# Kernel optimization log

Measured on AMD Instinct MI355X. Metric: run time of the kernel, lower is better.

## Reference

```python
import jax, jax.numpy as jnp
import numpy as np
from jax import lax

L, B, S, D, H = 4, 4, 2048, 1024, 2048
EPS = 1e-5


def setup_inputs() -> dict:
    key = jax.random.key(0)
    ks = jax.random.split(key, 8)

    def rn(k, shape, fan_in, fan_out):
        scale = (2.0 / (fan_in + fan_out)) ** 0.5  # xavier-ish
        return jax.random.normal(k, shape, jnp.float32) * scale

    return {
        "x": jax.random.normal(ks[0], (B, S, D), jnp.float32),
        "Wp1": rn(ks[1], (L, H, D), D, H),
        "bp1": jnp.zeros((L, H), jnp.float32),
        "Wp2": rn(ks[2], (L, H, D), D, H),
        "bp2": jnp.zeros((L, H), jnp.float32),
        "convW": rn(ks[3], (L, H, H, 3), 3 * H, H),  # torch Conv1d layout (O, I, K)
        "convb": jnp.zeros((L, H), jnp.float32),
        "Wz": rn(ks[4], (L, H, H), H, H),
        "bz": jnp.zeros((L, H), jnp.float32),
        "Wh": rn(ks[5], (L, H, H), H, H),
        "bh": jnp.zeros((L, H), jnp.float32),
        "Wd": rn(ks[6], (L, D, H), H, D),
        "bd": jnp.zeros((L, D), jnp.float32),
        # 4 LayerNorms per layer: [strand1_ln1, conv_ln, gru_ln, strand2_ln1]
        "ln_g": jnp.ones((L, 4, H), jnp.float32),
        "ln_b": jnp.zeros((L, 4, H), jnp.float32),
    }


def _ln(x, g, b):
    m = jnp.mean(x, axis=-1, keepdims=True)
    xc = x - m
    v = jnp.mean(xc * xc, axis=-1, keepdims=True)
    return xc * lax.rsqrt(v + EPS) * g + b


def _log_g(x):
    return jnp.where(x >= 0, jnp.log(jax.nn.relu(x) + 0.5), -jax.nn.softplus(-x))


def _min_gru(x, Wz, bz, Wh, bh):
    # x: (B, S, H); training-mode log-space parallel scan, h_0 = 0
    k = jnp.einsum('bsh,oh->bso', x, Wz) + bz
    log_z = -jax.nn.softplus(-k)
    log_coeffs = -jax.nn.softplus(k)
    log_h0 = jnp.full((x.shape[0], 1, Wz.shape[0]), jnp.log(0.5), x.dtype)  # log_g(0)
    log_tilde_h = _log_g(jnp.einsum('bsh,oh->bso', x, Wh) + bh)
    log_values = jnp.concatenate([log_h0, log_z + log_tilde_h], axis=1)  # (B,S+1,H)
    a_star = jnp.pad(jnp.cumsum(log_coeffs, axis=1), ((0, 0), (1, 0), (0, 0)))
    log_h = a_star + lax.cumlogsumexp(log_values - a_star, axis=1)
    return jnp.exp(log_h)[:, 1:]


def _conv1d(x, w, b):
    # x: (B, S, H) -> NCH conv with kernel 3, same padding
    y = lax.conv_general_dilated(
        x.transpose(0, 2, 1), w, window_strides=(1,), padding=((1, 1),),
        dimension_numbers=('NCH', 'OIH', 'NCH'))
    return (y + b[None, :, None]).transpose(0, 2, 1)


def _forward(x, Wp1, bp1, Wp2, bp2, convW, convb, Wz, bz, Wh, bh, Wd, bd, ln_g, ln_b):
    for i in range(L):
        s1 = _ln(jnp.einsum('bsd,hd->bsh', x, Wp1[i]) + bp1[i], ln_g[i, 0], ln_b[i, 0])
        s1 = _ln(_conv1d(s1, convW[i], convb[i]), ln_g[i, 1], ln_b[i, 1])
        s1 = jax.nn.silu(s1)
        s1 = _min_gru(s1, Wz[i], bz[i], Wh[i], bh[i])
        s1 = _ln(s1, ln_g[i, 2], ln_b[i, 2])
        s2 = jax.nn.silu(_ln(jnp.einsum('bsd,hd->bsh', x, Wp2[i]) + bp2[i], ln_g[i, 3], ln_b[i, 3]))
        x = jnp.einsum('bsh,dh->bsd', s1 * s2, Wd[i]) + bd[i] + x
    return x


def reference(x, Wp1, bp1, Wp2, bp2, convW, convb, Wz, bz, Wh, bh, Wd, bd, ln_g, ln_b):
    return _forward(x, Wp1, bp1, Wp2, bp2, convW, convb, Wz, bz, Wh, bh, Wd, bd, ln_g, ln_b)
```

## Files before the change

kernel.cpp:

```cpp
#include <hip/hip_runtime.h>

typedef unsigned short u16;
typedef short  s16x8 __attribute__((ext_vector_type(8)));
typedef float  f32x4 __attribute__((ext_vector_type(4)));
typedef unsigned short u16x4 __attribute__((ext_vector_type(4)));

#define LDS_AS __attribute__((address_space(3)))
#define GLB_AS __attribute__((address_space(1)))

__device__ __forceinline__ float bf2f(u16 x) {
    unsigned u = ((unsigned)x) << 16;
    return __builtin_bit_cast(float, u);
}
__device__ __forceinline__ u16 f2bf(float f) {
    unsigned u = __builtin_bit_cast(unsigned, f);
    return (u16)((u + 0x7FFFu + ((u >> 16) & 1u)) >> 16);
}
__device__ __forceinline__ void gload16(const u16* g, u16* l) {
    __builtin_amdgcn_global_load_lds((const GLB_AS unsigned int*)g,
                                     (LDS_AS unsigned int*)l, 16, 0, 0);
}

static constexpr int Lc = 4, Sc = 2048, Dc = 1024, Hc = 2048, Mc = 8192;
static constexpr int CH = 64, CL = 32;
static constexpr int NCHAN = 4 * Hc;

#define BAR() __builtin_amdgcn_s_barrier()
#define VMCNT(n) asm volatile("s_waitcnt vmcnt(" #n ")" ::: "memory")

#define READ_A(d, BUF, MH)                                                     \
    _Pragma("unroll") for (int mf = 0; mf < 4; ++mf) {                         \
        d[mf][0] = *(const s16x8*)(aB0 + (BUF)*16384 + (MH)*4096 + mf*1024);   \
        d[mf][1] = *(const s16x8*)(aB1 + (BUF)*16384 + (MH)*4096 + mf*1024);   \
    }
#define READ_B(BUF, NH)                                                        \
    _Pragma("unroll") for (int jb = 0; jb < 2; ++jb) {                         \
        bq[jb][0] = *(const s16x8*)(bB0 + (BUF)*16384 + (NH)*2048 + jb*1024);  \
        bq[jb][1] = *(const s16x8*)(bB1 + (BUF)*16384 + (NH)*2048 + jb*1024);  \
    }
#define QUAD(a, MH, NH)                                                        \
    _Pragma("unroll") for (int mf = 0; mf < 4; ++mf)                           \
    _Pragma("unroll") for (int jb = 0; jb < 2; ++jb)                           \
    _Pragma("unroll") for (int kk = 0; kk < 2; ++kk)                           \
        acc[(MH)*4 + mf][(NH)*2 + jb] = __builtin_amdgcn_mfma_f32_16x16x32_bf16( \
            a[mf][kk], bq[jb][kk], acc[(MH)*4 + mf][(NH)*2 + jb], 0, 0, 0);

#define STAGE_A(BUF, H, KT) {                                                  \
    if (CONV) {                                                                \
        const int seg_ = ((KT)*64) >> 11;                                      \
        const int kb_  = ((KT)*64) & (Hc - 1);                                 \
        const int r0_  = convRow + (H)*128 + seg_;                             \
        const u16* s0_ = ((unsigned)(r0_ - bb) < (unsigned)Sc)                 \
                             ? A + (size_t)r0_ * lda + kb_ + scol : zerobuf;   \
        const u16* s1_ = ((unsigned)(r0_ + 8 - bb) < (unsigned)Sc)             \
                             ? A + (size_t)(r0_ + 8) * lda + kb_ + scol : zerobuf; \
        gload16(s0_, ldsA + (BUF)*16384 + (H)*8192);                           \
        gload16(s1_, ldsA + (BUF)*16384 + (H)*8192 + 512);                     \
    } else {                                                                   \
        const u16* s_ = srcA + (size_t)((H)*128) * lda + (KT)*64;              \
        gload16(s_,                   ldsA + (BUF)*16384 + (H)*8192);          \
        gload16(s_ + 8*(size_t)lda,   ldsA + (BUF)*16384 + (H)*8192 + 512);    \
    } }
#define STAGE_B(BUF, H, KT) {                                                  \
    const u16* s_ = srcB + (size_t)((H)*128) * K + (KT)*64;                    \
    gload16(s_,                 ldsB + (BUF)*16384 + (H)*8192);                \
    gload16(s_ + 8*(size_t)K,   ldsB + (BUF)*16384 + (H)*8192 + 512);          \
}

template <int CONV>
__global__ __launch_bounds__(512, 2)
void gemm8(const u16* __restrict__ A, const u16* __restrict__ Bw,
           const float* __restrict__ bias, u16* __restrict__ Cb,
           int M, int N, int K, int lda, const u16* __restrict__ zerobuf) {
    (void)M;
    __shared__ __align__(16) u16 As[2][256][64];
    __shared__ __align__(16) u16 Bs[2][256][64];

    const int tid = threadIdx.x;
    const int w = tid >> 6, l = tid & 63;
    const int wm = w & 1, wn = w >> 1;
    const int rowBase = blockIdx.y * 256;
    const int colBase = blockIdx.x * 256;

    const int srow = w * 16 + (l >> 3);
    const int scol = ((l & 7) ^ (l >> 3)) << 3;
    const u16* srcB = Bw + (size_t)(colBase + srow) * K + scol;
    const u16* srcA = A + (size_t)(rowBase + srow) * lda + scol;
    u16* const ldsA = &As[0][0][0] + w * 1024;
    u16* const ldsB = &Bs[0][0][0] + w * 1024;
    const int bb = rowBase & ~(Sc - 1);
    const int convRow = rowBase + srow - 1;

    const int r16 = l & 15, slot = l >> 4;
    const int swz = (r16 & 7) << 4;
    const int co0 = (((slot << 4)      ) ^ swz) >> 1;
    const int co1 = (((slot << 4) | 64 ) ^ swz) >> 1;
    const u16* aB0 = &As[0][0][0] + (wm * 128 + r16) * 64 + co0;
    const u16* aB1 = &As[0][0][0] + (wm * 128 + r16) * 64 + co1;
    const u16* bB0 = &Bs[0][0][0] + (wn * 64  + r16) * 64 + co0;
    const u16* bB1 = &Bs[0][0][0] + (wn * 64  + r16) * 64 + co1;

    f32x4 acc[8][4];
#pragma unroll
    for (int m = 0; m < 8; ++m)
#pragma unroll
        for (int n = 0; n < 4; ++n)
#pragma unroll
            for (int r = 0; r < 4; ++r) acc[m][n][r] = 0.f;

    s16x8 a0[4][2], a1[4][2], bq[2][2];

    STAGE_A(0, 0, 0); STAGE_A(0, 1, 0); STAGE_B(0, 0, 0); STAGE_B(0, 1, 0);
    VMCNT(4);
    STAGE_A(1, 0, 1); STAGE_A(1, 1, 1); STAGE_B(1, 0, 1);
    VMCNT(6);
    BAR();

    const int NI = K >> 7;
    for (int i = 0; i < NI; ++i) {
        const int t1 = 2 * i + 1, t2 = 2 * i + 2, t3 = 2 * i + 3;
        const bool more = (i + 1 < NI);
        READ_A(a0, 0, 0); READ_B(0, 0);
        STAGE_B(1, 1, t1);
        BAR();
        __builtin_amdgcn_s_setprio(1); QUAD(a0, 0, 0); __builtin_amdgcn_s_setprio(0);
        BAR();
        READ_A(a1, 0, 1);
        BAR();
        __builtin_amdgcn_s_setprio(1); QUAD(a1, 1, 0); __builtin_amdgcn_s_setprio(0);
        BAR();
        READ_B(0, 1);
        if (more) { STAGE_A(0, 0, t2); STAGE_A(0, 1, t2); }
        BAR();
        __builtin_amdgcn_s_setprio(1); QUAD(a0, 0, 1); __builtin_amdgcn_s_setprio(0);
        BAR();
        if (more) STAGE_B(0, 0, t2);
        BAR();
        __builtin_amdgcn_s_setprio(1); QUAD(a1, 1, 1); __builtin_amdgcn_s_setprio(0);
        if (more) { VMCNT(6); } else { VMCNT(0); }
        BAR();
        READ_A(a0, 1, 0); READ_B(1, 0);
        if (more) STAGE_B(0, 1, t2);
        BAR();
        __builtin_amdgcn_s_setprio(1); QUAD(a0, 0, 0); __builtin_amdgcn_s_setprio(0);
        BAR();
        READ_A(a1, 1, 1);
        BAR();
        __builtin_amdgcn_s_setprio(1); QUAD(a1, 1, 0); __builtin_amdgcn_s_setprio(0);
        BAR();
        READ_B(1, 1);
        if (more) { STAGE_A(1, 0, t3); STAGE_A(1, 1, t3); }
        BAR();
        __builtin_amdgcn_s_setprio(1); QUAD(a0, 0, 1); __builtin_amdgcn_s_setprio(0);
        BAR();
        if (more) STAGE_B(1, 0, t3);
        BAR();
        __builtin_amdgcn_s_setprio(1); QUAD(a1, 1, 1); __builtin_amdgcn_s_setprio(0);
        if (more) VMCNT(6);
        BAR();
    }

    const int coll  = colBase + wn * 64 + r16;
    const int row00 = rowBase + wm * 128 + slot * 4;
#pragma unroll
    for (int m8 = 0; m8 < 8; ++m8) {
#pragma unroll
        for (int n4 = 0; n4 < 4; ++n4) {
            const int col = coll + n4 * 16;
            const float bv = bias[col];
            const int row0 = row00 + m8 * 16;
#pragma unroll
            for (int r = 0; r < 4; ++r)
                Cb[(size_t)(row0 + r) * N + col] = f2bf(acc[m8][n4][r] + bv);
        }
    }
}

template <int CONV, int EPI>
__global__ __launch_bounds__(256)
void gemm_bt(const u16* __restrict__ A, const u16* __restrict__ Bw,
             const float* __restrict__ bias,
             u16* __restrict__ Cb, float* __restrict__ Cf,
             const float* __restrict__ resid, u16* __restrict__ xout,
             int M, int N, int K, int lda, const u16* __restrict__ zerobuf) {
    __shared__ __align__(16) u16 As[128 * 32];
    __shared__ __align__(16) u16 Bs[128 * 32];
    const int tid  = threadIdx.x;
    const int wave = tid >> 6, lane = tid & 63;
    const int rowBase = blockIdx.y * 128;
    const int colBase = blockIdx.x * 128;
    const int srow = tid >> 2;
    const int scol = (tid & 3) << 3;

    u16* ldsA0 = As + wave * 512;
    u16* ldsA1 = As + 2048 + wave * 512;
    u16* ldsB0 = Bs + wave * 512;
    u16* ldsB1 = Bs + 2048 + wave * 512;

    const u16* bpt0 = Bw + (size_t)(colBase + srow) * K + scol;
    const u16* bpt1 = Bw + (size_t)(colBase + 64 + srow) * K + scol;
    const int arow0 = rowBase + srow;
    const int arow1 = arow0 + 64;
    const u16* ap0 = A + (size_t)arow0 * lda + scol;
    const u16* ap1 = A + (size_t)arow1 * lda + scol;

    const int wm = wave & 1, wn = wave >> 1;
    const int mB = wm * 64, nB = wn * 64;
    const int quad = lane >> 4, l16 = lane & 15;

    f32x4 acc[4][4];
#pragma unroll
    for (int a = 0; a < 4; a++)
#pragma unroll
        for (int b = 0; b < 4; b++)
#pragma unroll
            for (int r = 0; r < 4; r++) acc[a][b][r] = 0.f;

    for (int k0 = 0; k0 < K; k0 += 32) {
        if (CONV) {
            const int seg = k0 >> 11;
            const int kk  = (k0 & (Hc - 1)) + scol;
            const int bbb = rowBase & ~(Sc - 1);
            const int r0  = arow0 + seg - 1;
            const int r1  = arow1 + seg - 1;
            const u16* g0 = ((unsigned)(r0 - bbb) < (unsigned)Sc) ? A + (size_t)r0 * lda + kk : zerobuf;
            const u16* g1 = ((unsigned)(r1 - bbb) < (unsigned)Sc) ? A + (size_t)r1 * lda + kk : zerobuf;
            gload16(g0, ldsA0);
            gload16(g1, ldsA1);
        } else {
            gload16(ap0 + k0, ldsA0);
            gload16(ap1 + k0, ldsA1);
        }
        gload16(bpt0 + k0, ldsB0);
        gload16(bpt1 + k0, ldsB1);
        __syncthreads();

        s16x8 af[4], bfr[4];
#pragma unroll
        for (int t = 0; t < 4; t++)
            af[t] = *(const s16x8*)(As + (mB + t * 16 + l16) * 32 + (quad << 3));
#pragma unroll
        for (int t = 0; t < 4; t++)
            bfr[t] = *(const s16x8*)(Bs + (nB + t * 16 + l16) * 32 + (quad << 3));
#pragma unroll
        for (int mt = 0; mt < 4; mt++)
#pragma unroll
            for (int nt = 0; nt < 4; nt++)
                acc[mt][nt] = __builtin_amdgcn_mfma_f32_16x16x32_bf16(af[mt], bfr[nt], acc[mt][nt], 0, 0, 0);
        __syncthreads();
    }

#pragma unroll
    for (int mt = 0; mt < 4; mt++) {
#pragma unroll
        for (int nt = 0; nt < 4; nt++) {
            const int col  = colBase + nB + nt * 16 + l16;
            const int row0 = rowBase + mB + mt * 16 + (quad << 2);
            const float bv = bias[col];
#pragma unroll
            for (int r = 0; r < 4; r++) {
                const size_t idx = (size_t)(row0 + r) * N + col;
                float v = acc[mt][nt][r] + bv;
                if (EPI == 0) {
                    Cb[idx] = f2bf(v);
                } else {
                    v += resid[idx];
                    Cf[idx]   = v;
                    xout[idx] = f2bf(v);
                }
            }
        }
    }
}

__global__ __launch_bounds__(256)
void ln_fuse(const u16* __restrict__ in, u16* __restrict__ out,
             const float* __restrict__ g, const float* __restrict__ b,
             const u16* __restrict__ mul, int do_silu) {
    __shared__ float sred[4], qred[4];
    const int row = blockIdx.x, tid = threadIdx.x;
    const int lane = tid & 63, wave = tid >> 6;
    const size_t base = (size_t)row * Hc + tid * 8;

    s16x8 v8 = *(const s16x8*)(in + base);
    float x[8];
#pragma unroll
    for (int j = 0; j < 8; j++) x[j] = bf2f((u16)v8[j]);
    float s = 0.f, q = 0.f;
#pragma unroll
    for (int j = 0; j < 8; j++) { s += x[j]; q += x[j] * x[j]; }
#pragma unroll
    for (int off = 32; off > 0; off >>= 1) {
        s += __shfl_down(s, off);
        q += __shfl_down(q, off);
    }
    if (lane == 0) { sred[wave] = s; qred[wave] = q; }
    __syncthreads();
    const float St = sred[0] + sred[1] + sred[2] + sred[3];
    const float Qt = qred[0] + qred[1] + qred[2] + qred[3];
    const float mean = St * (1.0f / Hc);
    const float var  = Qt * (1.0f / Hc) - mean * mean;
    const float rs   = rsqrtf(var + 1e-5f);

    const int c = tid * 8;
    const float4 g0 = *(const float4*)(g + c), g1 = *(const float4*)(g + c + 4);
    const float4 b0 = *(const float4*)(b + c), b1 = *(const float4*)(b + c + 4);
    const float gg[8] = {g0.x, g0.y, g0.z, g0.w, g1.x, g1.y, g1.z, g1.w};
    const float bb[8] = {b0.x, b0.y, b0.z, b0.w, b1.x, b1.y, b1.z, b1.w};
    s16x8 m8;
    if (mul) m8 = *(const s16x8*)(mul + base);
    s16x8 o8;
#pragma unroll
    for (int j = 0; j < 8; j++) {
        float y = (x[j] - mean) * rs * gg[j] + bb[j];
        if (do_silu) y = y / (1.0f + __expf(-y));
        if (mul) y *= bf2f((u16)m8[j]);
        o8[j] = (short)f2bf(y);
    }
    *(s16x8*)(out + base) = o8;
}

__device__ __forceinline__ void scan_step(float k, float p, float& ct, float& vt) {
    const float l1p = __logf(1.f + __expf(-fabsf(k)));
    ct = -(fmaxf(k, 0.f) + l1p);
    const float lg = (p >= 0.f) ? __logf(p + 0.5f)
                                : -(fmaxf(-p, 0.f) + __logf(1.f + __expf(-fabsf(p))));
    vt = -(fmaxf(-k, 0.f) + l1p) + lg;
}
__device__ __forceinline__ float laddexp(float a, float b) {
    const float m = fmaxf(a, b);
    return m + __logf(1.f + __expf(-fabsf(a - b)));
}

__global__ __launch_bounds__(256)
void scan_part1(const u16* __restrict__ kb, const u16* __restrict__ pb,
                float* __restrict__ Cc, float* __restrict__ Vv) {
    const int tid = threadIdx.x;
    const int hb = blockIdx.x & 7;
    const int c  = (blockIdx.x >> 3) & 63;
    const int b  = blockIdx.x >> 9;
    const int h  = hb * 256 + tid;
    size_t idx = (size_t)b * Sc * Hc + (size_t)(c * CL) * Hc + h;
    float C = 0.f, V = -1e30f;
#pragma unroll 4
    for (int t = 0; t < CL; t++) {
        float ct, vt;
        scan_step(bf2f(kb[idx]), bf2f(pb[idx]), ct, vt);
        V = laddexp(V + ct, vt);
        C += ct;
        idx += Hc;
    }
    const int chan = b * Hc + h;
    Cc[c * NCHAN + chan] = C;
    Vv[c * NCHAN + chan] = V;
}

__global__ __launch_bounds__(256)
void scan_mid(const float* __restrict__ Cc, const float* __restrict__ Vv,
              float* __restrict__ carry) {
    const int chan = blockIdx.x * 256 + threadIdx.x;
    float lh = -0.69314718f;
    for (int c = 0; c < CH; c++) {
        carry[c * NCHAN + chan] = lh;
        lh = laddexp(lh + Cc[c * NCHAN + chan], Vv[c * NCHAN + chan]);
    }
}

__global__ __launch_bounds__(256)
void scan_part3(const u16* __restrict__ kb, const u16* __restrict__ pb,
                const float* __restrict__ carry, u16* __restrict__ out) {
    const int tid = threadIdx.x;
    const int hb = blockIdx.x & 7;
    const int c  = (blockIdx.x >> 3) & 63;
    const int b  = blockIdx.x >> 9;
    const int h  = hb * 256 + tid;
    size_t idx = (size_t)b * Sc * Hc + (size_t)(c * CL) * Hc + h;
    float lh = carry[c * NCHAN + (b * Hc + h)];
#pragma unroll 4
    for (int t = 0; t < CL; t++) {
        float ct, vt;
        scan_step(bf2f(kb[idx]), bf2f(pb[idx]), ct, vt);
        lh = laddexp(lh + ct, vt);
        out[idx] = f2bf(__expf(lh));
        idx += Hc;
    }
}

__global__ __launch_bounds__(256)
void castf2b(const float* __restrict__ in, u16* __restrict__ out, int n) {
    const int i = (blockIdx.x * 256 + threadIdx.x) << 2;
    if (i >= n) return;
    const float4 v = *(const float4*)(in + i);
    u16x4 o;
    o.x = f2bf(v.x); o.y = f2bf(v.y); o.z = f2bf(v.z); o.w = f2bf(v.w);
    *(u16x4*)(out + i) = o;
}

__global__ __launch_bounds__(256)
void conv_tr(const float* __restrict__ w, u16* __restrict__ out) {
    const int idx = blockIdx.x * 256 + threadIdx.x;
    const float* src = w + (size_t)idx * 3;
    const float a = src[0], b = src[1], c = src[2];
    const int o = idx >> 11, ii = idx & (Hc - 1);
    u16* dst = out + (size_t)o * (3 * Hc) + ii;
    dst[0]        = f2bf(a);
    dst[Hc]       = f2bf(b);
    dst[2 * Hc]   = f2bf(c);
}

static inline void launch_gemm8(int conv, const u16* A, const u16* Bw,
                                const float* bias, u16* C,
                                int M, int N, int K, int lda,
                                const u16* zero, hipStream_t s) {
    dim3 grid(N / 256, M / 256), blk(512);
    if (conv) gemm8<1><<<grid, blk, 0, s>>>(A, Bw, bias, C, M, N, K, lda, zero);
    else      gemm8<0><<<grid, blk, 0, s>>>(A, Bw, bias, C, M, N, K, lda, zero);
}

extern "C" void kernel_launch(void* const* d_in, const int* in_sizes, int n_in,
                              void* d_out, int out_size, void* d_ws, size_t ws_size,
                              hipStream_t stream) {
    (void)in_sizes; (void)n_in; (void)out_size; (void)ws_size;
    const float* x0    = (const float*)d_in[0];
    const float* Wp1   = (const float*)d_in[1];
    const float* bp1   = (const float*)d_in[2];
    const float* Wp2   = (const float*)d_in[3];
    const float* bp2   = (const float*)d_in[4];
    const float* convW = (const float*)d_in[5];
    const float* convb = (const float*)d_in[6];
    const float* Wz    = (const float*)d_in[7];
    const float* bz    = (const float*)d_in[8];
    const float* Wh    = (const float*)d_in[9];
    const float* bh    = (const float*)d_in[10];
    const float* Wd    = (const float*)d_in[11];
    const float* bd    = (const float*)d_in[12];
    const float* lng   = (const float*)d_in[13];
    const float* lnb   = (const float*)d_in[14];
    float* out = (float*)d_out;

    char* ws = (char*)d_ws;
    u16* wbuf = (u16*)(ws);
    u16* s1   = (u16*)(ws + 25165824);
    u16* t1   = (u16*)(ws + 58720256);
    u16* s2   = (u16*)(ws + 92274688);
    u16* pbuf = (u16*)(ws + 125829120);
    u16* xb   = (u16*)(ws + 159383552);
    u16* zero = (u16*)(ws + 176160768);
    float* scanC = (float*)(ws + 176161792);
    float* scanV = (float*)(ws + 178258944);
    float* carry = (float*)(ws + 180356096);

    hipMemsetAsync(zero, 0, 1024, stream);
    castf2b<<<dim3((Mc * Dc / 4) / 256), dim3(256), 0, stream>>>(x0, xb, Mc * Dc);

    const size_t wpStride = (size_t)Hc * Dc;
    const size_t cvStride = (size_t)Hc * Hc * 3;
    const size_t wzStride = (size_t)Hc * Hc;
    const size_t wdStride = (size_t)Dc * Hc;

    for (int i = 0; i < Lc; ++i) {
        const float* g0 = lng + ((size_t)i * 4 + 0) * Hc; const float* be0 = lnb + ((size_t)i * 4 + 0) * Hc;
        const float* g1 = lng + ((size_t)i * 4 + 1) * Hc; const float* be1 = lnb + ((size_t)i * 4 + 1) * Hc;
        const float* g2 = lng + ((size_t)i * 4 + 2) * Hc; const float* be2 = lnb + ((size_t)i * 4 + 2) * Hc;
        const float* g3 = lng + ((size_t)i * 4 + 3) * Hc; const float* be3 = lnb + ((size_t)i * 4 + 3) * Hc;

        castf2b<<<dim3((int)(wpStride / 4 / 256)), dim3(256), 0, stream>>>(Wp1 + i * wpStride, wbuf, (int)wpStride);
        launch_gemm8(0, xb, wbuf, bp1 + (size_t)i * Hc, t1, Mc, Hc, Dc, Dc, zero, stream);
        ln_fuse<<<dim3(Mc), dim3(256), 0, stream>>>(t1, s1, g0, be0, nullptr, 0);

        conv_tr<<<dim3((Hc * Hc) / 256), dim3(256), 0, stream>>>(convW + i * cvStride, wbuf);
        launch_gemm8(1, s1, wbuf, convb + (size_t)i * Hc, t1, Mc, Hc, 3 * Hc, Hc, zero, stream);
        ln_fuse<<<dim3(Mc), dim3(256), 0, stream>>>(t1, s1, g1, be1, nullptr, 1);

        castf2b<<<dim3((int)(wzStride / 4 / 256)), dim3(256), 0, stream>>>(Wz + i * wzStride, wbuf, (int)wzStride);
        launch_gemm8(0, s1, wbuf, bz + (size_t)i * Hc, s2, Mc, Hc, Hc, Hc, zero, stream);
        castf2b<<<dim3((int)(wzStride / 4 / 256)), dim3(256), 0, stream>>>(Wh + i * wzStride, wbuf, (int)wzStride);
        launch_gemm8(0, s1, wbuf, bh + (size_t)i * Hc, pbuf, Mc, Hc, Hc, Hc, zero, stream);
        scan_part1<<<dim3(2048), dim3(256), 0, stream>>>(s2, pbuf, scanC, scanV);
        scan_mid<<<dim3(32), dim3(256), 0, stream>>>(scanC, scanV, carry);
        scan_part3<<<dim3(2048), dim3(256), 0, stream>>>(s2, pbuf, carry, t1);
        ln_fuse<<<dim3(Mc), dim3(256), 0, stream>>>(t1, s1, g2, be2, nullptr, 0);

        castf2b<<<dim3((int)(wpStride / 4 / 256)), dim3(256), 0, stream>>>(Wp2 + i * wpStride, wbuf, (int)wpStride);
        launch_gemm8(0, xb, wbuf, bp2 + (size_t)i * Hc, t1, Mc, Hc, Dc, Dc, zero, stream);
        ln_fuse<<<dim3(Mc), dim3(256), 0, stream>>>(t1, s2, g3, be3, s1, 1);

        castf2b<<<dim3((int)(wdStride / 4 / 256)), dim3(256), 0, stream>>>(Wd + i * wdStride, wbuf, (int)wdStride);
        gemm_bt<0, 1><<<dim3(Dc / 128, Mc / 128), dim3(256), 0, stream>>>(
            s2, wbuf, bd + (size_t)i * Dc, nullptr, out,
            (i == 0) ? x0 : out, xb, Mc, Dc, Hc, Hc, zero);
    }
}
```

Measured before the change: 3.027 ms.

## Fuse Wz/Wh GEMMs, swizzle workgroup order, route down-projection through gemm8

```diff
diff --git a/kernel.cpp b/kernel.cpp
--- a/kernel.cpp
+++ b/kernel.cpp
@@ -24,6 +24,7 @@
 static constexpr int Lc = 4, Sc = 2048, Dc = 1024, Hc = 2048, Mc = 8192;
 static constexpr int CH = 64, CL = 32;
 static constexpr int NCHAN = 4 * Hc;
+static constexpr int KPW = 4096;
 
 #define BAR() __builtin_amdgcn_s_barrier()
 #define VMCNT(n) asm volatile("s_waitcnt vmcnt(" #n ")" ::: "memory")
@@ -67,10 +68,12 @@
     gload16(s_ + 8*(size_t)K,   ldsB + (BUF)*16384 + (H)*8192 + 512);          \
 }
 
-template <int CONV>
+template <int CONV, int EPI>
 __global__ __launch_bounds__(512, 2)
 void gemm8(const u16* __restrict__ A, const u16* __restrict__ Bw,
            const float* __restrict__ bias, u16* __restrict__ Cb,
+           float* __restrict__ Cf, const float* __restrict__ resid,
+           u16* __restrict__ xout,
            int M, int N, int K, int lda, const u16* __restrict__ zerobuf) {
     (void)M;
     __shared__ __align__(16) u16 As[2][256][64];
@@ -79,8 +82,14 @@
     const int tid = threadIdx.x;
     const int w = tid >> 6, l = tid & 63;
     const int wm = w & 1, wn = w >> 1;
-    const int rowBase = blockIdx.y * 256;
-    const int colBase = blockIdx.x * 256;
+
+    const unsigned nwg = gridDim.x * gridDim.y;
+    unsigned id = blockIdx.x + gridDim.x * blockIdx.y;
+    id = (id & 7u) * (nwg >> 3) + (id >> 3);
+    const int bx = (int)(id % gridDim.x);
+    const int by = (int)(id / gridDim.x);
+    const int rowBase = by * 256;
+    const int colBase = bx * 256;
 
     const int srow = w * 16 + (l >> 3);
     const int scol = ((l & 7) ^ (l >> 3)) << 3;
@@ -170,97 +179,9 @@
             const float bv = bias[col];
             const int row0 = row00 + m8 * 16;
 #pragma unroll
-            for (int r = 0; r < 4; ++r)
-                Cb[(size_t)(row0 + r) * N + col] = f2bf(acc[m8][n4][r] + bv);
-        }
-    }
-}
-
-template <int CONV, int EPI>
-__global__ __launch_bounds__(256)
-void gemm_bt(const u16* __restrict__ A, const u16* __restrict__ Bw,
-             const float* __restrict__ bias,
-             u16* __restrict__ Cb, float* __restrict__ Cf,
-             const float* __restrict__ resid, u16* __restrict__ xout,
-             int M, int N, int K, int lda, const u16* __restrict__ zerobuf) {
-    __shared__ __align__(16) u16 As[128 * 32];
-    __shared__ __align__(16) u16 Bs[128 * 32];
-    const int tid  = threadIdx.x;
-    const int wave = tid >> 6, lane = tid & 63;
-    const int rowBase = blockIdx.y * 128;
-    const int colBase = blockIdx.x * 128;
-    const int srow = tid >> 2;
-    const int scol = (tid & 3) << 3;
-
-    u16* ldsA0 = As + wave * 512;
-    u16* ldsA1 = As + 2048 + wave * 512;
-    u16* ldsB0 = Bs + wave * 512;
-    u16* ldsB1 = Bs + 2048 + wave * 512;
-
-    const u16* bpt0 = Bw + (size_t)(colBase + srow) * K + scol;
-    const u16* bpt1 = Bw + (size_t)(colBase + 64 + srow) * K + scol;
-    const int arow0 = rowBase + srow;
-    const int arow1 = arow0 + 64;
-    const u16* ap0 = A + (size_t)arow0 * lda + scol;
-    const u16* ap1 = A + (size_t)arow1 * lda + scol;
-
-    const int wm = wave & 1, wn = wave >> 1;
-    const int mB = wm * 64, nB = wn * 64;
-    const int quad = lane >> 4, l16 = lane & 15;
-
-    f32x4 acc[4][4];
-#pragma unroll
-    for (int a = 0; a < 4; a++)
-#pragma unroll
-        for (int b = 0; b < 4; b++)
-#pragma unroll
-            for (int r = 0; r < 4; r++) acc[a][b][r] = 0.f;
-
-    for (int k0 = 0; k0 < K; k0 += 32) {
-        if (CONV) {
-            const int seg = k0 >> 11;
-            const int kk  = (k0 & (Hc - 1)) + scol;
-            const int bbb = rowBase & ~(Sc - 1);
-            const int r0  = arow0 + seg - 1;
-            const int r1  = arow1 + seg - 1;
-            const u16* g0 = ((unsigned)(r0 - bbb) < (unsigned)Sc) ? A + (size_t)r0 * lda + kk : zerobuf;
-            const u16* g1 = ((unsigned)(r1 - bbb) < (unsigned)Sc) ? A + (size_t)r1 * lda + kk : zerobuf;
-            gload16(g0, ldsA0);
-            gload16(g1, ldsA1);
-        } else {
-            gload16(ap0 + k0, ldsA0);
-            gload16(ap1 + k0, ldsA1);
-        }
-        gload16(bpt0 + k0, ldsB0);
-        gload16(bpt1 + k0, ldsB1);
-        __syncthreads();
-
-        s16x8 af[4], bfr[4];
-#pragma unroll
-        for (int t = 0; t < 4; t++)
-            af[t] = *(const s16x8*)(As + (mB + t * 16 + l16) * 32 + (quad << 3));
-#pragma unroll
-        for (int t = 0; t < 4; t++)
-            bfr[t] = *(const s16x8*)(Bs + (nB + t * 16 + l16) * 32 + (quad << 3));
-#pragma unroll
-        for (int mt = 0; mt < 4; mt++)
-#pragma unroll
-            for (int nt = 0; nt < 4; nt++)
-                acc[mt][nt] = __builtin_amdgcn_mfma_f32_16x16x32_bf16(af[mt], bfr[nt], acc[mt][nt], 0, 0, 0);
-        __syncthreads();
-    }
-
-#pragma unroll
-    for (int mt = 0; mt < 4; mt++) {
-#pragma unroll
-        for (int nt = 0; nt < 4; nt++) {
-            const int col  = colBase + nB + nt * 16 + l16;
-            const int row0 = rowBase + mB + mt * 16 + (quad << 2);
-            const float bv = bias[col];
-#pragma unroll
-            for (int r = 0; r < 4; r++) {
+            for (int r = 0; r < 4; ++r) {
                 const size_t idx = (size_t)(row0 + r) * N + col;
-                float v = acc[mt][nt][r] + bv;
+                float v = acc[m8][n4][r] + bv;
                 if (EPI == 0) {
                     Cb[idx] = f2bf(v);
                 } else {
@@ -333,22 +254,22 @@
 }
 
 __global__ __launch_bounds__(256)
-void scan_part1(const u16* __restrict__ kb, const u16* __restrict__ pb,
+void scan_part1(const u16* __restrict__ kp,
                 float* __restrict__ Cc, float* __restrict__ Vv) {
     const int tid = threadIdx.x;
     const int hb = blockIdx.x & 7;
     const int c  = (blockIdx.x >> 3) & 63;
     const int b  = blockIdx.x >> 9;
     const int h  = hb * 256 + tid;
-    size_t idx = (size_t)b * Sc * Hc + (size_t)(c * CL) * Hc + h;
+    size_t idx = (size_t)(b * Sc + c * CL) * KPW + h;
     float C = 0.f, V = -1e30f;
 #pragma unroll 4
     for (int t = 0; t < CL; t++) {
         float ct, vt;
-        scan_step(bf2f(kb[idx]), bf2f(pb[idx]), ct, vt);
+        scan_step(bf2f(kp[idx]), bf2f(kp[idx + Hc]), ct, vt);
         V = laddexp(V + ct, vt);
         C += ct;
-        idx += Hc;
+        idx += KPW;
     }
     const int chan = b * Hc + h;
     Cc[c * NCHAN + chan] = C;
@@ -367,22 +288,24 @@
 }
 
 __global__ __launch_bounds__(256)
-void scan_part3(const u16* __restrict__ kb, const u16* __restrict__ pb,
+void scan_part3(const u16* __restrict__ kp,
                 const float* __restrict__ carry, u16* __restrict__ out) {
     const int tid = threadIdx.x;
     const int hb = blockIdx.x & 7;
     const int c  = (blockIdx.x >> 3) & 63;
     const int b  = blockIdx.x >> 9;
     const int h  = hb * 256 + tid;
-    size_t idx = (size_t)b * Sc * Hc + (size_t)(c * CL) * Hc + h;
+    size_t idx = (size_t)(b * Sc + c * CL) * KPW + h;
+    size_t odx = (size_t)(b * Sc + c * CL) * Hc + h;
     float lh = carry[c * NCHAN + (b * Hc + h)];
 #pragma unroll 4
     for (int t = 0; t < CL; t++) {
         float ct, vt;
-        scan_step(bf2f(kb[idx]), bf2f(pb[idx]), ct, vt);
+        scan_step(bf2f(kp[idx]), bf2f(kp[idx + Hc]), ct, vt);
         lh = laddexp(lh + ct, vt);
-        out[idx] = f2bf(__expf(lh));
-        idx += Hc;
+        out[odx] = f2bf(__expf(lh));
+        idx += KPW;
+        odx += Hc;
     }
 }
 
@@ -408,13 +331,18 @@
     dst[2 * Hc]   = f2bf(c);
 }
 
-static inline void launch_gemm8(int conv, const u16* A, const u16* Bw,
-                                const float* bias, u16* C,
+static inline void launch_gemm8(int conv, int epi,
+                                const u16* A, const u16* Bw, const float* bias,
+                                u16* Cb, float* Cf, const float* resid, u16* xout,
                                 int M, int N, int K, int lda,
                                 const u16* zero, hipStream_t s) {
     dim3 grid(N / 256, M / 256), blk(512);
-    if (conv) gemm8<1><<<grid, blk, 0, s>>>(A, Bw, bias, C, M, N, K, lda, zero);
-    else      gemm8<0><<<grid, blk, 0, s>>>(A, Bw, bias, C, M, N, K, lda, zero);
+    if (conv)
+        gemm8<1, 0><<<grid, blk, 0, s>>>(A, Bw, bias, Cb, Cf, resid, xout, M, N, K, lda, zero);
+    else if (epi)
+        gemm8<0, 1><<<grid, blk, 0, s>>>(A, Bw, bias, Cb, Cf, resid, xout, M, N, K, lda, zero);
+    else
+        gemm8<0, 0><<<grid, blk, 0, s>>>(A, Bw, bias, Cb, Cf, resid, xout, M, N, K, lda, zero);
 }
 
 extern "C" void kernel_launch(void* const* d_in, const int* in_sizes, int n_in,
@@ -442,13 +370,14 @@
     u16* wbuf = (u16*)(ws);
     u16* s1   = (u16*)(ws + 25165824);
     u16* t1   = (u16*)(ws + 58720256);
-    u16* s2   = (u16*)(ws + 92274688);
-    u16* pbuf = (u16*)(ws + 125829120);
+    u16* kp   = (u16*)(ws + 92274688);
+    u16* s2   = kp;
     u16* xb   = (u16*)(ws + 159383552);
     u16* zero = (u16*)(ws + 176160768);
     float* scanC = (float*)(ws + 176161792);
     float* scanV = (float*)(ws + 178258944);
     float* carry = (float*)(ws + 180356096);
+    float* bias2 = (float*)(ws + 182453248);
 
     hipMemsetAsync(zero, 0, 1024, stream);
     castf2b<<<dim3((Mc * Dc / 4) / 256), dim3(256), 0, stream>>>(x0, xb, Mc * Dc);
@@ -465,29 +394,33 @@
         const float* g3 = lng + ((size_t)i * 4 + 3) * Hc; const float* be3 = lnb + ((size_t)i * 4 + 3) * Hc;
 
         castf2b<<<dim3((int)(wpStride / 4 / 256)), dim3(256), 0, stream>>>(Wp1 + i * wpStride, wbuf, (int)wpStride);
-        launch_gemm8(0, xb, wbuf, bp1 + (size_t)i * Hc, t1, Mc, Hc, Dc, Dc, zero, stream);
+        launch_gemm8(0, 0, xb, wbuf, bp1 + (size_t)i * Hc, t1, nullptr, nullptr, nullptr,
+                     Mc, Hc, Dc, Dc, zero, stream);
         ln_fuse<<<dim3(Mc), dim3(256), 0, stream>>>(t1, s1, g0, be0, nullptr, 0);
 
         conv_tr<<<dim3((Hc * Hc) / 256), dim3(256), 0, stream>>>(convW + i * cvStride, wbuf);
-        launch_gemm8(1, s1, wbuf, convb + (size_t)i * Hc, t1, Mc, Hc, 3 * Hc, Hc, zero, stream);
+        launch_gemm8(1, 0, s1, wbuf, convb + (size_t)i * Hc, t1, nullptr, nullptr, nullptr,
+                     Mc, Hc, 3 * Hc, Hc, zero, stream);
         ln_fuse<<<dim3(Mc), dim3(256), 0, stream>>>(t1, s1, g1, be1, nullptr, 1);
 
         castf2b<<<dim3((int)(wzStride / 4 / 256)), dim3(256), 0, stream>>>(Wz + i * wzStride, wbuf, (int)wzStride);
-        launch_gemm8(0, s1, wbuf, bz + (size_t)i * Hc, s2, Mc, Hc, Hc, Hc, zero, stream);
-        castf2b<<<dim3((int)(wzStride / 4 / 256)), dim3(256), 0, stream>>>(Wh + i * wzStride, wbuf, (int)wzStride);
-        launch_gemm8(0, s1, wbuf, bh + (size_t)i * Hc, pbuf, Mc, Hc, Hc, Hc, zero, stream);
-        scan_part1<<<dim3(2048), dim3(256), 0, stream>>>(s2, pbuf, scanC, scanV);
+        castf2b<<<dim3((int)(wzStride / 4 / 256)), dim3(256), 0, stream>>>(Wh + i * wzStride, wbuf + wzStride, (int)wzStride);
+        hipMemcpyAsync(bias2,        bz + (size_t)i * Hc, Hc * sizeof(float), hipMemcpyDeviceToDevice, stream);
+        hipMemcpyAsync(bias2 + Hc,   bh + (size_t)i * Hc, Hc * sizeof(float), hipMemcpyDeviceToDevice, stream);
+        launch_gemm8(0, 0, s1, wbuf, bias2, kp, nullptr, nullptr, nullptr,
+                     Mc, KPW, Hc, Hc, zero, stream);
+        scan_part1<<<dim3(2048), dim3(256), 0, stream>>>(kp, scanC, scanV);
         scan_mid<<<dim3(32), dim3(256), 0, stream>>>(scanC, scanV, carry);
-        scan_part3<<<dim3(2048), dim3(256), 0, stream>>>(s2, pbuf, carry, t1);
+        scan_part3<<<dim3(2048), dim3(256), 0, stream>>>(kp, carry, t1);
         ln_fuse<<<dim3(Mc), dim3(256), 0, stream>>>(t1, s1, g2, be2, nullptr, 0);
 
         castf2b<<<dim3((int)(wpStride / 4 / 256)), dim3(256), 0, stream>>>(Wp2 + i * wpStride, wbuf, (int)wpStride);
-        launch_gemm8(0, xb, wbuf, bp2 + (size_t)i * Hc, t1, Mc, Hc, Dc, Dc, zero, stream);
+        launch_gemm8(0, 0, xb, wbuf, bp2 + (size_t)i * Hc, t1, nullptr, nullptr, nullptr,
+                     Mc, Hc, Dc, Dc, zero, stream);
         ln_fuse<<<dim3(Mc), dim3(256), 0, stream>>>(t1, s2, g3, be3, s1, 1);
 
         castf2b<<<dim3((int)(wdStride / 4 / 256)), dim3(256), 0, stream>>>(Wd + i * wdStride, wbuf, (int)wdStride);
-        gemm_bt<0, 1><<<dim3(Dc / 128, Mc / 128), dim3(256), 0, stream>>>(
-            s2, wbuf, bd + (size_t)i * Dc, nullptr, out,
-            (i == 0) ? x0 : out, xb, Mc, Dc, Hc, Hc, zero);
-    }
-}
+        launch_gemm8(0, 1, s2, wbuf, bd + (size_t)i * Dc, nullptr, out,
+                     (i == 0) ? x0 : out, xb, Mc, Dc, Hc, Hc, zero, stream);
+    }
+}
```

Result: faster. 2.942 ms (-2.8%).

## Concatenate paired GEMM weights, add persistent row reps and XCD-aware block remap

Applied to the files above, without the earlier changes.

```diff
diff --git a/kernel.cpp b/kernel.cpp
--- a/kernel.cpp
+++ b/kernel.cpp
@@ -24,6 +24,7 @@
 static constexpr int Lc = 4, Sc = 2048, Dc = 1024, Hc = 2048, Mc = 8192;
 static constexpr int CH = 64, CL = 32;
 static constexpr int NCHAN = 4 * Hc;
+static constexpr int KPW = 4096;
 
 #define BAR() __builtin_amdgcn_s_barrier()
 #define VMCNT(n) asm volatile("s_waitcnt vmcnt(" #n ")" ::: "memory")
@@ -67,7 +68,7 @@
     gload16(s_ + 8*(size_t)K,   ldsB + (BUF)*16384 + (H)*8192 + 512);          \
 }
 
-template <int CONV>
+template <int CONV, int REPS>
 __global__ __launch_bounds__(512, 2)
 void gemm8(const u16* __restrict__ A, const u16* __restrict__ Bw,
            const float* __restrict__ bias, u16* __restrict__ Cb,
@@ -79,17 +80,19 @@
     const int tid = threadIdx.x;
     const int w = tid >> 6, l = tid & 63;
     const int wm = w & 1, wn = w >> 1;
-    const int rowBase = blockIdx.y * 256;
-    const int colBase = blockIdx.x * 256;
+
+    const unsigned nwg = gridDim.x * gridDim.y;
+    unsigned id = blockIdx.x + gridDim.x * blockIdx.y;
+    id = (id & 7u) * (nwg >> 3) + (id >> 3);
+    const int bx = (int)(id % gridDim.x);
+    const int byBase = (int)(id / gridDim.x);
+    const int colBase = bx * 256;
 
     const int srow = w * 16 + (l >> 3);
     const int scol = ((l & 7) ^ (l >> 3)) << 3;
     const u16* srcB = Bw + (size_t)(colBase + srow) * K + scol;
-    const u16* srcA = A + (size_t)(rowBase + srow) * lda + scol;
     u16* const ldsA = &As[0][0][0] + w * 1024;
     u16* const ldsB = &Bs[0][0][0] + w * 1024;
-    const int bb = rowBase & ~(Sc - 1);
-    const int convRow = rowBase + srow - 1;
 
     const int r16 = l & 15, slot = l >> 4;
     const int swz = (r16 & 7) << 4;
@@ -100,78 +103,86 @@
     const u16* bB0 = &Bs[0][0][0] + (wn * 64  + r16) * 64 + co0;
     const u16* bB1 = &Bs[0][0][0] + (wn * 64  + r16) * 64 + co1;
 
-    f32x4 acc[8][4];
-#pragma unroll
-    for (int m = 0; m < 8; ++m)
-#pragma unroll
-        for (int n = 0; n < 4; ++n)
-#pragma unroll
-            for (int r = 0; r < 4; ++r) acc[m][n][r] = 0.f;
-
-    s16x8 a0[4][2], a1[4][2], bq[2][2];
-
-    STAGE_A(0, 0, 0); STAGE_A(0, 1, 0); STAGE_B(0, 0, 0); STAGE_B(0, 1, 0);
-    VMCNT(4);
-    STAGE_A(1, 0, 1); STAGE_A(1, 1, 1); STAGE_B(1, 0, 1);
-    VMCNT(6);
-    BAR();
-
-    const int NI = K >> 7;
-    for (int i = 0; i < NI; ++i) {
-        const int t1 = 2 * i + 1, t2 = 2 * i + 2, t3 = 2 * i + 3;
-        const bool more = (i + 1 < NI);
-        READ_A(a0, 0, 0); READ_B(0, 0);
-        STAGE_B(1, 1, t1);
+    const int coll = colBase + wn * 64 + r16;
+
+    for (int rep = 0; rep < REPS; ++rep) {
+        const int rowBase = (byBase + rep * gridDim.y) * 256;
+        const u16* srcA = A + (size_t)(rowBase + srow) * lda + scol;
+        const int bb = rowBase & ~(Sc - 1);
+        const int convRow = rowBase + srow - 1;
+
+        f32x4 acc[8][4];
+#pragma unroll
+        for (int m = 0; m < 8; ++m)
+#pragma unroll
+            for (int n = 0; n < 4; ++n)
+#pragma unroll
+                for (int r = 0; r < 4; ++r) acc[m][n][r] = 0.f;
+
+        s16x8 a0[4][2], a1[4][2], bq[2][2];
+
+        STAGE_A(0, 0, 0); STAGE_A(0, 1, 0); STAGE_B(0, 0, 0); STAGE_B(0, 1, 0);
+        VMCNT(4);
+        STAGE_A(1, 0, 1); STAGE_A(1, 1, 1); STAGE_B(1, 0, 1);
+        VMCNT(6);
         BAR();
-        __builtin_amdgcn_s_setprio(1); QUAD(a0, 0, 0); __builtin_amdgcn_s_setprio(0);
-        BAR();
-        READ_A(a1, 0, 1);
-        BAR();
-        __builtin_amdgcn_s_setprio(1); QUAD(a1, 1, 0); __builtin_amdgcn_s_setprio(0);
-        BAR();
-        READ_B(0, 1);
-        if (more) { STAGE_A(0, 0, t2); STAGE_A(0, 1, t2); }
-        BAR();
-        __builtin_amdgcn_s_setprio(1); QUAD(a0, 0, 1); __builtin_amdgcn_s_setprio(0);
-        BAR();
-        if (more) STAGE_B(0, 0, t2);
-        BAR();
-        __builtin_amdgcn_s_setprio(1); QUAD(a1, 1, 1); __builtin_amdgcn_s_setprio(0);
-        if (more) { VMCNT(6); } else { VMCNT(0); }
-        BAR();
-        READ_A(a0, 1, 0); READ_B(1, 0);
-        if (more) STAGE_B(0, 1, t2);
-        BAR();
-        __builtin_amdgcn_s_setprio(1); QUAD(a0, 0, 0); __builtin_amdgcn_s_setprio(0);
-        BAR();
-        READ_A(a1, 1, 1);
-        BAR();
-        __builtin_amdgcn_s_setprio(1); QUAD(a1, 1, 0); __builtin_amdgcn_s_setprio(0);
-        BAR();
-        READ_B(1, 1);
-        if (more) { STAGE_A(1, 0, t3); STAGE_A(1, 1, t3); }
-        BAR();
-        __builtin_amdgcn_s_setprio(1); QUAD(a0, 0, 1); __builtin_amdgcn_s_setprio(0);
-        BAR();
-        if (more) STAGE_B(1, 0, t3);
-        BAR();
-        __builtin_amdgcn_s_setprio(1); QUAD(a1, 1, 1); __builtin_amdgcn_s_setprio(0);
-        if (more) VMCNT(6);
-        BAR();
-    }
-
-    const int coll  = colBase + wn * 64 + r16;
-    const int row00 = rowBase + wm * 128 + slot * 4;
-#pragma unroll
-    for (int m8 = 0; m8 < 8; ++m8) {
-#pragma unroll
-        for (int n4 = 0; n4 < 4; ++n4) {
-            const int col = coll + n4 * 16;
-            const float bv = bias[col];
-            const int row0 = row00 + m8 * 16;
-#pragma unroll
-            for (int r = 0; r < 4; ++r)
-                Cb[(size_t)(row0 + r) * N + col] = f2bf(acc[m8][n4][r] + bv);
+
+        const int NI = K >> 7;
+        for (int i = 0; i < NI; ++i) {
+            const int t1 = 2 * i + 1, t2 = 2 * i + 2, t3 = 2 * i + 3;
+            const bool more = (i + 1 < NI);
+            READ_A(a0, 0, 0); READ_B(0, 0);
+            STAGE_B(1, 1, t1);
+            BAR();
+            __builtin_amdgcn_s_setprio(1); QUAD(a0, 0, 0); __builtin_amdgcn_s_setprio(0);
+            BAR();
+            READ_A(a1, 0, 1);
+            BAR();
+            __builtin_amdgcn_s_setprio(1); QUAD(a1, 1, 0); __builtin_amdgcn_s_setprio(0);
+            BAR();
+            READ_B(0, 1);
+            if (more) { STAGE_A(0, 0, t2); STAGE_A(0, 1, t2); }
+            BAR();
+            __builtin_amdgcn_s_setprio(1); QUAD(a0, 0, 1); __builtin_amdgcn_s_setprio(0);
+            BAR();
+            if (more) STAGE_B(0, 0, t2);
+            BAR();
+            __builtin_amdgcn_s_setprio(1); QUAD(a1, 1, 1); __builtin_amdgcn_s_setprio(0);
+            if (more) { VMCNT(6); } else { VMCNT(0); }
+            BAR();
+            READ_A(a0, 1, 0); READ_B(1, 0);
+            if (more) STAGE_B(0, 1, t2);
+            BAR();
+            __builtin_amdgcn_s_setprio(1); QUAD(a0, 0, 0); __builtin_amdgcn_s_setprio(0);
+            BAR();
+            READ_A(a1, 1, 1);
+            BAR();
+            __builtin_amdgcn_s_setprio(1); QUAD(a1, 1, 0); __builtin_amdgcn_s_setprio(0);
+            BAR();
+            READ_B(1, 1);
+            if (more) { STAGE_A(1, 0, t3); STAGE_A(1, 1, t3); }
+            BAR();
+            __builtin_amdgcn_s_setprio(1); QUAD(a0, 0, 1); __builtin_amdgcn_s_setprio(0);
+            BAR();
+            if (more) STAGE_B(1, 0, t3);
+            BAR();
+            __builtin_amdgcn_s_setprio(1); QUAD(a1, 1, 1); __builtin_amdgcn_s_setprio(0);
+            if (more) VMCNT(6);
+            BAR();
+        }
+
+        const int row00 = rowBase + wm * 128 + slot * 4;
+#pragma unroll
+        for (int m8 = 0; m8 < 8; ++m8) {
+#pragma unroll
+            for (int n4 = 0; n4 < 4; ++n4) {
+                const int col = coll + n4 * 16;
+                const float bv = bias[col];
+                const int row0 = row00 + m8 * 16;
+#pragma unroll
+                for (int r = 0; r < 4; ++r)
+                    Cb[(size_t)(row0 + r) * N + col] = f2bf(acc[m8][n4][r] + bv);
+            }
         }
     }
 }
@@ -274,15 +285,16 @@
 }
 
 __global__ __launch_bounds__(256)
-void ln_fuse(const u16* __restrict__ in, u16* __restrict__ out,
+void ln_fuse(const u16* __restrict__ in, int instride, u16* __restrict__ out,
              const float* __restrict__ g, const float* __restrict__ b,
              const u16* __restrict__ mul, int do_silu) {
     __shared__ float sred[4], qred[4];
     const int row = blockIdx.x, tid = threadIdx.x;
     const int lane = tid & 63, wave = tid >> 6;
-    const size_t base = (size_t)row * Hc + tid * 8;
-
-    s16x8 v8 = *(const s16x8*)(in + base);
+    const size_t ibase = (size_t)row * instride + tid * 8;
+    const size_t obase = (size_t)row * Hc + tid * 8;
+
+    s16x8 v8 = *(const s16x8*)(in + ibase);
     float x[8];
 #pragma unroll
     for (int j = 0; j < 8; j++) x[j] = bf2f((u16)v8[j]);
@@ -308,7 +320,7 @@
     const float gg[8] = {g0.x, g0.y, g0.z, g0.w, g1.x, g1.y, g1.z, g1.w};
     const float bb[8] = {b0.x, b0.y, b0.z, b0.w, b1.x, b1.y, b1.z, b1.w};
     s16x8 m8;
-    if (mul) m8 = *(const s16x8*)(mul + base);
+    if (mul) m8 = *(const s16x8*)(mul + obase);
     s16x8 o8;
 #pragma unroll
     for (int j = 0; j < 8; j++) {
@@ -317,7 +329,7 @@
         if (mul) y *= bf2f((u16)m8[j]);
         o8[j] = (short)f2bf(y);
     }
-    *(s16x8*)(out + base) = o8;
+    *(s16x8*)(out + obase) = o8;
 }
 
 __device__ __forceinline__ void scan_step(float k, float p, float& ct, float& vt) {
@@ -333,22 +345,22 @@
 }
 
 __global__ __launch_bounds__(256)
-void scan_part1(const u16* __restrict__ kb, const u16* __restrict__ pb,
+void scan_part1(const u16* __restrict__ kp,
                 float* __restrict__ Cc, float* __restrict__ Vv) {
     const int tid = threadIdx.x;
     const int hb = blockIdx.x & 7;
     const int c  = (blockIdx.x >> 3) & 63;
     const int b  = blockIdx.x >> 9;
     const int h  = hb * 256 + tid;
-    size_t idx = (size_t)b * Sc * Hc + (size_t)(c * CL) * Hc + h;
+    size_t idx = (size_t)(b * Sc + c * CL) * KPW + h;
     float C = 0.f, V = -1e30f;
 #pragma unroll 4
     for (int t = 0; t < CL; t++) {
         float ct, vt;
-        scan_step(bf2f(kb[idx]), bf2f(pb[idx]), ct, vt);
+        scan_step(bf2f(kp[idx]), bf2f(kp[idx + Hc]), ct, vt);
         V = laddexp(V + ct, vt);
         C += ct;
-        idx += Hc;
+        idx += KPW;
     }
     const int chan = b * Hc + h;
     Cc[c * NCHAN + chan] = C;
@@ -360,29 +372,40 @@
               float* __restrict__ carry) {
     const int chan = blockIdx.x * 256 + threadIdx.x;
     float lh = -0.69314718f;
-    for (int c = 0; c < CH; c++) {
-        carry[c * NCHAN + chan] = lh;
-        lh = laddexp(lh + Cc[c * NCHAN + chan], Vv[c * NCHAN + chan]);
-    }
-}
-
-__global__ __launch_bounds__(256)
-void scan_part3(const u16* __restrict__ kb, const u16* __restrict__ pb,
+    for (int cb = 0; cb < CH; cb += 8) {
+        float Cr[8], Vr[8];
+#pragma unroll
+        for (int j = 0; j < 8; j++) {
+            Cr[j] = Cc[(cb + j) * NCHAN + chan];
+            Vr[j] = Vv[(cb + j) * NCHAN + chan];
+        }
+#pragma unroll
+        for (int j = 0; j < 8; j++) {
+            carry[(cb + j) * NCHAN + chan] = lh;
+            lh = laddexp(lh + Cr[j], Vr[j]);
+        }
+    }
+}
+
+__global__ __launch_bounds__(256)
+void scan_part3(const u16* __restrict__ kp,
                 const float* __restrict__ carry, u16* __restrict__ out) {
     const int tid = threadIdx.x;
     const int hb = blockIdx.x & 7;
     const int c  = (blockIdx.x >> 3) & 63;
     const int b  = blockIdx.x >> 9;
     const int h  = hb * 256 + tid;
-    size_t idx = (size_t)b * Sc * Hc + (size_t)(c * CL) * Hc + h;
+    size_t idx = (size_t)(b * Sc + c * CL) * KPW + h;
+    size_t odx = (size_t)(b * Sc + c * CL) * Hc + h;
     float lh = carry[c * NCHAN + (b * Hc + h)];
 #pragma unroll 4
     for (int t = 0; t < CL; t++) {
         float ct, vt;
-        scan_step(bf2f(kb[idx]), bf2f(pb[idx]), ct, vt);
+        scan_step(bf2f(kp[idx]), bf2f(kp[idx + Hc]), ct, vt);
         lh = laddexp(lh + ct, vt);
-        out[idx] = f2bf(__expf(lh));
-        idx += Hc;
+        out[odx] = f2bf(__expf(lh));
+        idx += KPW;
+        odx += Hc;
     }
 }
 
@@ -394,6 +417,27 @@
     u16x4 o;
     o.x = f2bf(v.x); o.y = f2bf(v.y); o.z = f2bf(v.z); o.w = f2bf(v.w);
     *(u16x4*)(out + i) = o;
+}
+
+__global__ __launch_bounds__(256)
+void prep2(const float* __restrict__ srcA, const float* __restrict__ srcB,
+           const float* __restrict__ bA, const float* __restrict__ bB,
+           u16* __restrict__ dst, float* __restrict__ bias_dst, int nPerHalf) {
+    const int bid = blockIdx.x, tid = threadIdx.x;
+    const int halfBlocks = gridDim.x >> 1;
+    const int half = (bid >= halfBlocks) ? 1 : 0;
+    const size_t i = ((size_t)(bid - half * halfBlocks) * 256 + tid) * 4;
+    const float* src = half ? srcB : srcA;
+    const float4 v = *(const float4*)(src + i);
+    u16x4 o;
+    o.x = f2bf(v.x); o.y = f2bf(v.y); o.z = f2bf(v.z); o.w = f2bf(v.w);
+    *(u16x4*)(dst + (size_t)half * nPerHalf + i) = o;
+    if (bid < 4) {
+        const int j = bid * 1024 + tid * 4;
+        const float4 vb = (j < 2048) ? *(const float4*)(bA + j)
+                                     : *(const float4*)(bB + (j - 2048));
+        *(float4*)(bias_dst + j) = vb;
+    }
 }
 
 __global__ __launch_bounds__(256)
@@ -408,19 +452,10 @@
     dst[2 * Hc]   = f2bf(c);
 }
 
-static inline void launch_gemm8(int conv, const u16* A, const u16* Bw,
-                                const float* bias, u16* C,
-                                int M, int N, int K, int lda,
-                                const u16* zero, hipStream_t s) {
-    dim3 grid(N / 256, M / 256), blk(512);
-    if (conv) gemm8<1><<<grid, blk, 0, s>>>(A, Bw, bias, C, M, N, K, lda, zero);
-    else      gemm8<0><<<grid, blk, 0, s>>>(A, Bw, bias, C, M, N, K, lda, zero);
-}
-
 extern "C" void kernel_launch(void* const* d_in, const int* in_sizes, int n_in,
                               void* d_out, int out_size, void* d_ws, size_t ws_size,
                               hipStream_t stream) {
-    (void)in_sizes; (void)n_in; (void)out_size; (void)ws_size;
+    (void)in_sizes; (void)n_in; (void)out_size;
     const float* x0    = (const float*)d_in[0];
     const float* Wp1   = (const float*)d_in[1];
     const float* bp1   = (const float*)d_in[2];
@@ -442,13 +477,16 @@
     u16* wbuf = (u16*)(ws);
     u16* s1   = (u16*)(ws + 25165824);
     u16* t1   = (u16*)(ws + 58720256);
-    u16* s2   = (u16*)(ws + 92274688);
-    u16* pbuf = (u16*)(ws + 125829120);
+    u16* kp   = (u16*)(ws + 92274688);
+    u16* s2   = kp;
     u16* xb   = (u16*)(ws + 159383552);
     u16* zero = (u16*)(ws + 176160768);
     float* scanC = (float*)(ws + 176161792);
     float* scanV = (float*)(ws + 178258944);
     float* carry = (float*)(ws + 180356096);
+    float* bias2 = (float*)(ws + 182453248);
+    u16* P       = (u16*)(ws + 184549376);
+    const bool FUSEP = ws_size >= 251658240ull;
 
     hipMemsetAsync(zero, 0, 1024, stream);
     castf2b<<<dim3((Mc * Dc / 4) / 256), dim3(256), 0, stream>>>(x0, xb, Mc * Dc);
@@ -464,30 +502,50 @@
         const float* g2 = lng + ((size_t)i * 4 + 2) * Hc; const float* be2 = lnb + ((size_t)i * 4 + 2) * Hc;
         const float* g3 = lng + ((size_t)i * 4 + 3) * Hc; const float* be3 = lnb + ((size_t)i * 4 + 3) * Hc;
 
-        castf2b<<<dim3((int)(wpStride / 4 / 256)), dim3(256), 0, stream>>>(Wp1 + i * wpStride, wbuf, (int)wpStride);
-        launch_gemm8(0, xb, wbuf, bp1 + (size_t)i * Hc, t1, Mc, Hc, Dc, Dc, zero, stream);
-        ln_fuse<<<dim3(Mc), dim3(256), 0, stream>>>(t1, s1, g0, be0, nullptr, 0);
+        if (FUSEP) {
+            prep2<<<dim3(2 * (int)(wpStride / 1024)), dim3(256), 0, stream>>>(
+                Wp1 + i * wpStride, Wp2 + i * wpStride,
+                bp1 + (size_t)i * Hc, bp2 + (size_t)i * Hc, wbuf, bias2, (int)wpStride);
+            gemm8<0, 2><<<dim3(KPW / 256, Mc / 512), dim3(512), 0, stream>>>(
+                xb, wbuf, bias2, P, Mc, KPW, Dc, Dc, zero);
+            ln_fuse<<<dim3(Mc), dim3(256), 0, stream>>>(P, KPW, s1, g0, be0, nullptr, 0);
+        } else {
+            castf2b<<<dim3((int)(wpStride / 4 / 256)), dim3(256), 0, stream>>>(Wp1 + i * wpStride, wbuf, (int)wpStride);
+            gemm8<0, 2><<<dim3(Hc / 256, Mc / 512), dim3(512), 0, stream>>>(
+                xb, wbuf, bp1 + (size_t)i * Hc, t1, Mc, Hc, Dc, Dc, zero);
+            ln_fuse<<<dim3(Mc), dim3(256), 0, stream>>>(t1, Hc, s1, g0, be0, nullptr, 0);
+        }
 
         conv_tr<<<dim3((Hc * Hc) / 256), dim3(256), 0, stream>>>(convW + i * cvStride, wbuf);
-        launch_gemm8(1, s1, wbuf, convb + (size_t)i * Hc, t1, Mc, Hc, 3 * Hc, Hc, zero, stream);
-        ln_fuse<<<dim3(Mc), dim3(256), 0, stream>>>(t1, s1, g1, be1, nullptr, 1);
-
-        castf2b<<<dim3((int)(wzStride / 4 / 256)), dim3(256), 0, stream>>>(Wz + i * wzStride, wbuf, (int)wzStride);
-        launch_gemm8(0, s1, wbuf, bz + (size_t)i * Hc, s2, Mc, Hc, Hc, Hc, zero, stream);
-        castf2b<<<dim3((int)(wzStride / 4 / 256)), dim3(256), 0, stream>>>(Wh + i * wzStride, wbuf, (int)wzStride);
-        launch_gemm8(0, s1, wbuf, bh + (size_t)i * Hc, pbuf, Mc, Hc, Hc, Hc, zero, stream);
-        scan_part1<<<dim3(2048), dim3(256), 0, stream>>>(s2, pbuf, scanC, scanV);
+        gemm8<1, 1><<<dim3(Hc / 256, Mc / 256), dim3(512), 0, stream>>>(
+            s1, wbuf, convb + (size_t)i * Hc, t1, Mc, Hc, 3 * Hc, Hc, zero);
+        ln_fuse<<<dim3(Mc), dim3(256), 0, stream>>>(t1, Hc, s1, g1, be1, nullptr, 1);
+
+        prep2<<<dim3(2 * (int)(wzStride / 1024)), dim3(256), 0, stream>>>(
+            Wz + i * wzStride, Wh + i * wzStride,
+            bz + (size_t)i * Hc, bh + (size_t)i * Hc, wbuf, bias2, (int)wzStride);
+        gemm8<0, 2><<<dim3(KPW / 256, Mc / 512), dim3(512), 0, stream>>>(
+            s1, wbuf, bias2, kp, Mc, KPW, Hc, Hc, zero);
+        scan_part1<<<dim3(2048), dim3(256), 0, stream>>>(kp, scanC, scanV);
         scan_mid<<<dim3(32), dim3(256), 0, stream>>>(scanC, scanV, carry);
-        scan_part3<<<dim3(2048), dim3(256), 0, stream>>>(s2, pbuf, carry, t1);
-        ln_fuse<<<dim3(Mc), dim3(256), 0, stream>>>(t1, s1, g2, be2, nullptr, 0);
-
-        castf2b<<<dim3((int)(wpStride / 4 / 256)), dim3(256), 0, stream>>>(Wp2 + i * wpStride, wbuf, (int)wpStride);
-        launch_gemm8(0, xb, wbuf, bp2 + (size_t)i * Hc, t1, Mc, Hc, Dc, Dc, zero, stream);
-        ln_fuse<<<dim3(Mc), dim3(256), 0, stream>>>(t1, s2, g3, be3, s1, 1);
-
-        castf2b<<<dim3((int)(wdStride / 4 / 256)), dim3(256), 0, stream>>>(Wd + i * wdStride, wbuf, (int)wdStride);
-        gemm_bt<0, 1><<<dim3(Dc / 128, Mc / 128), dim3(256), 0, stream>>>(
-            s2, wbuf, bd + (size_t)i * Dc, nullptr, out,
-            (i == 0) ? x0 : out, xb, Mc, Dc, Hc, Hc, zero);
-    }
-}
+        scan_part3<<<dim3(2048), dim3(256), 0, stream>>>(kp, carry, t1);
+        ln_fuse<<<dim3(Mc), dim3(256), 0, stream>>>(t1, Hc, s1, g2, be2, nullptr, 0);
+
+        if (FUSEP) {
+            ln_fuse<<<dim3(Mc), dim3(256), 0, stream>>>(P + Hc, KPW, t1, g3, be3, s1, 1);
+            castf2b<<<dim3((int)(wdStride / 4 / 256)), dim3(256), 0, stream>>>(Wd + i * wdStride, wbuf, (int)wdStride);
+            gemm_bt<0, 1><<<dim3(Dc / 128, Mc / 128), dim3(256), 0, stream>>>(
+                t1, wbuf, bd + (size_t)i * Dc, nullptr, out,
+                (i == 0) ? x0 : out, xb, Mc, Dc, Hc, Hc, zero);
+        } else {
+            castf2b<<<dim3((int)(wpStride / 4 / 256)), dim3(256), 0, stream>>>(Wp2 + i * wpStride, wbuf, (int)wpStride);
+            gemm8<0, 2><<<dim3(Hc / 256, Mc / 512), dim3(512), 0, stream>>>(
+                xb, wbuf, bp2 + (size_t)i * Hc, t1, Mc, Hc, Dc, Dc, zero);
+            ln_fuse<<<dim3(Mc), dim3(256), 0, stream>>>(t1, Hc, s2, g3, be3, s1, 1);
+            castf2b<<<dim3((int)(wdStride / 4 / 256)), dim3(256), 0, stream>>>(Wd + i * wdStride, wbuf, (int)wdStride);
+            gemm_bt<0, 1><<<dim3(Dc / 128, Mc / 128), dim3(256), 0, stream>>>(
+                s2, wbuf, bd + (size_t)i * Dc, nullptr, out,
+                (i == 0) ? x0 : out, xb, Mc, Dc, Hc, Hc, zero);
+        }
+    }
+}
```

Result: faster. 2.877 ms (-5.0%).
